# Optimization experiments

Measured on AMD Instinct MI355X. Metric: run time of the kernel, lower is better.

## Reference

```python
import jax, jax.numpy as jnp
import numpy as np

B, F, H, C = 256, 512, 1024, 1000
LN_EPS = 1e-5


def _proj(x, W, b, g, be):
    # AdaptiveAvgPool2d(1) + Flatten + Linear + LayerNorm + GELU(exact)
    p = x.mean(axis=(2, 3))                       # [B, Cin]
    h = p @ W + b                                 # [B, F]
    mu = h.mean(axis=-1, keepdims=True)
    var = h.var(axis=-1, keepdims=True)           # ddof=0, matches torch LayerNorm
    h = (h - mu) / jnp.sqrt(var + LN_EPS) * g + be
    return jax.nn.gelu(h, approximate=False)


def setup_inputs() -> dict:
    key = jax.random.key(0)
    ks = iter(jax.random.split(key, 64))
    def rn(shape, s=1.0):
        return jax.random.normal(next(ks), shape, jnp.float32) * s
    inp = {}
    feats = {"s1": (16, 112), "s2": (24, 56), "s3": (40, 28), "s4": (80, 14), "s5": (160, 7)}
    for n, (c, hw) in feats.items():
        inp[n] = rn((B, c, hw, hw))
    inp["ff"] = rn((B, 960, 7, 7))
    for i, c in enumerate([16, 24, 40, 80, 160], start=1):
        inp[f"Wp{i}"] = rn((c, F), 0.02)
        inp[f"bp{i}"] = jnp.zeros((F,), jnp.float32)
        inp[f"g{i}"] = jnp.ones((F,), jnp.float32)
        inp[f"be{i}"] = jnp.zeros((F,), jnp.float32)
    inp["Wg1"] = rn((960, H), 0.02); inp["bg1"] = jnp.zeros((H,), jnp.float32)
    inp["Wg2"] = rn((H, H // 2), 0.02); inp["bg2"] = jnp.zeros((H // 2,), jnp.float32)
    inp["Wg3"] = rn((H // 2, 5), 0.02); inp["bg3"] = jnp.zeros((5,), jnp.float32)
    inp["Wc1"] = rn((F, H), 0.02); inp["bc1"] = jnp.zeros((H,), jnp.float32)
    inp["Wc2"] = rn((H, H // 2), 0.02); inp["bc2"] = jnp.zeros((H // 2,), jnp.float32)
    inp["Wc3"] = rn((H // 2, C), 0.02); inp["bc3"] = jnp.zeros((C,), jnp.float32)
    return inp


def reference(s1, s2, s3, s4, s5, ff,
              Wp1, bp1, g1, be1, Wp2, bp2, g2, be2, Wp3, bp3, g3, be3,
              Wp4, bp4, g4, be4, Wp5, bp5, g5, be5,
              Wg1, bg1, Wg2, bg2, Wg3, bg3,
              Wc1, bc1, Wc2, bc2, Wc3, bc3):
    # gate on pooled final backbone features (dropout inactive at eval)
    gate_in = ff.mean(axis=(2, 3))                         # [B, 960]
    h = jax.nn.relu(gate_in @ Wg1 + bg1)
    h = jax.nn.relu(h @ Wg2 + bg2)
    gate_logits = h @ Wg3 + bg3                            # [B, 5]

    # per-stage projections -> [B, 5, F]
    stack = jnp.stack([
        _proj(s1, Wp1, bp1, g1, be1),
        _proj(s2, Wp2, bp2, g2, be2),
        _proj(s3, Wp3, bp3, g3, be3),
        _proj(s4, Wp4, bp4, g4, be4),
        _proj(s5, Wp5, bp5, g5, be5),
    ], axis=1)

    topv, topi = jax.lax.top_k(gate_logits, 2)             # [B, 2]
    w = jax.nn.softmax(topv, axis=1)                       # softmax over top-k logits
    sel = jnp.take_along_axis(stack, topi[:, :, None], axis=1)  # [B, 2, F]
    mixture = (sel * w[:, :, None]).sum(axis=1)            # [B, F]

    h = jax.nn.relu(mixture @ Wc1 + bc1)
    h = jax.nn.relu(h @ Wc2 + bc2)
    logits = h @ Wc3 + bc3                                 # [B, C]
    return logits, gate_logits, topi, w
```

## Files before the change

kernel.cpp:

```cpp
#include <hip/hip_runtime.h>
#include <math.h>


struct Pool4Segs {
    const float* src[4];
    float*       dst[4];
    int n4[4];
    int cum[4];
    float inv[4];
};

__global__ __launch_bounds__(256) void pool_big_kernel(Pool4Segs S, int total_waves) {
    int gid  = blockIdx.x * 256 + threadIdx.x;
    int wave = gid >> 6;
    int lane = gid & 63;
    if (wave >= total_waves) return;
    int s = 0;
    #pragma unroll
    for (int i = 0; i < 3; ++i) if (wave >= S.cum[i]) s = i + 1;
    int row = wave - (s == 0 ? 0 : S.cum[s - 1]);
    const int n4 = S.n4[s];
    const float4* p4 = (const float4*)(S.src[s]) + (size_t)row * n4;

    float a0 = 0.f, a1 = 0.f, a2 = 0.f, a3 = 0.f;
    float a4 = 0.f, a5 = 0.f, a6 = 0.f, a7 = 0.f;
    int k = lane;
    for (; k + 448 < n4; k += 512) {
        float4 v0 = p4[k];       float4 v1 = p4[k + 64];
        float4 v2 = p4[k + 128]; float4 v3 = p4[k + 192];
        float4 v4 = p4[k + 256]; float4 v5 = p4[k + 320];
        float4 v6 = p4[k + 384]; float4 v7 = p4[k + 448];
        a0 += (v0.x + v0.y) + (v0.z + v0.w);
        a1 += (v1.x + v1.y) + (v1.z + v1.w);
        a2 += (v2.x + v2.y) + (v2.z + v2.w);
        a3 += (v3.x + v3.y) + (v3.z + v3.w);
        a4 += (v4.x + v4.y) + (v4.z + v4.w);
        a5 += (v5.x + v5.y) + (v5.z + v5.w);
        a6 += (v6.x + v6.y) + (v6.z + v6.w);
        a7 += (v7.x + v7.y) + (v7.z + v7.w);
    }
    for (; k + 192 < n4; k += 256) {
        float4 v0 = p4[k];       float4 v1 = p4[k + 64];
        float4 v2 = p4[k + 128]; float4 v3 = p4[k + 192];
        a0 += (v0.x + v0.y) + (v0.z + v0.w);
        a1 += (v1.x + v1.y) + (v1.z + v1.w);
        a2 += (v2.x + v2.y) + (v2.z + v2.w);
        a3 += (v3.x + v3.y) + (v3.z + v3.w);
    }
    for (; k < n4; k += 64) {
        float4 v = p4[k];
        a0 += (v.x + v.y) + (v.z + v.w);
    }
    float acc = ((a0 + a1) + (a2 + a3)) + ((a4 + a5) + (a6 + a7));
    #pragma unroll
    for (int off = 32; off > 0; off >>= 1) acc += __shfl_down(acc, off, 64);
    if (lane == 0) S.dst[s][row] = acc * S.inv[s];
}

__global__ __launch_bounds__(256) void pool_small_kernel(const float* __restrict__ s5,
        const float* __restrict__ ff, float* __restrict__ dst5, float* __restrict__ dstf,
        int rows5) {
    __shared__ float lds[64 * 49];
    const int tid  = threadIdx.x;
    const int row0 = blockIdx.x * 64;
    const float* src;
    float* dst;
    int rbase;
    if (row0 < rows5) { src = s5; dst = dst5; rbase = row0; }
    else              { src = ff; dst = dstf; rbase = row0 - rows5; }
    const float4* p4 = (const float4*)(src + (size_t)rbase * 49);
    float4* l4 = (float4*)lds;
    float4 v0 = p4[tid];
    float4 v1 = p4[tid + 256];
    float4 v2 = p4[tid + 512];
    float4 v3;
    const bool t3 = (tid < 784 - 768);
    if (t3) v3 = p4[tid + 768];
    l4[tid]       = v0;
    l4[tid + 256] = v1;
    l4[tid + 512] = v2;
    if (t3) l4[tid + 768] = v3;
    __syncthreads();
    const int r  = tid >> 2;
    const int c0 = tid & 3;
    float s = 0.f;
    #pragma unroll
    for (int c = c0; c < 49; c += 4) s += lds[r * 49 + c];
    s += __shfl_down(s, 2, 64);
    s += __shfl_down(s, 1, 64);
    if (c0 == 0) dst[rbase + r] = s * (1.f / 49.f);
}

__global__ __launch_bounds__(256) void fc_tile_kernel(const float* __restrict__ X,
        const float* __restrict__ W, float* __restrict__ P,
        int M, int K, int N, int Kc, int ntiles) {
    __shared__ __align__(16) float Xs[8][68];
    __shared__ __align__(16) float Ws[8][68];
    const int tpk = 4 * ntiles;
    int bid = blockIdx.x;
    int ks  = bid / tpk;
    int rem = bid - ks * tpk;
    int mt  = rem / ntiles;
    int nt  = rem - mt * ntiles;
    const int m0 = mt * 64, n0 = nt * 64;
    const int k0 = ks * Kc;
    int k1 = k0 + Kc; if (k1 > K) k1 = K;

    const int tid = threadIdx.x;
    const int tm = tid & 15;
    const int tn = tid >> 4;
    const int xa = tid >> 3, xb = tid & 7;
    const int wc = tid & 63, wb = tid >> 6;
    const int nw = n0 + wc;
    const bool wok = (nw < N);

    float4 acc[4];
    #pragma unroll
    for (int r = 0; r < 4; ++r) acc[r] = make_float4(0.f, 0.f, 0.f, 0.f);

    float x0, x1, w0v, w1v;
    x0  = X[(size_t)(m0 + xa) * K + k0 + xb];
    x1  = X[(size_t)(m0 + xa + 32) * K + k0 + xb];
    w0v = wok ? W[(size_t)(k0 + wb) * N + nw] : 0.f;
    w1v = wok ? W[(size_t)(k0 + wb + 4) * N + nw] : 0.f;

    for (int kt = k0; kt < k1; kt += 8) {
        __syncthreads();
        Xs[xb][xa] = x0; Xs[xb][xa + 32] = x1;
        Ws[wb][wc] = w0v; Ws[wb + 4][wc] = w1v;
        __syncthreads();
        if (kt + 8 < k1) {
            x0  = X[(size_t)(m0 + xa) * K + kt + 8 + xb];
            x1  = X[(size_t)(m0 + xa + 32) * K + kt + 8 + xb];
            w0v = wok ? W[(size_t)(kt + 8 + wb) * N + nw] : 0.f;
            w1v = wok ? W[(size_t)(kt + 8 + wb + 4) * N + nw] : 0.f;
        }
        #pragma unroll
        for (int kk = 0; kk < 8; ++kk) {
            float4 xr = *(const float4*)&Xs[kk][tm * 4];
            float4 wr = *(const float4*)&Ws[kk][tn * 4];
            acc[0].x += xr.x * wr.x; acc[0].y += xr.x * wr.y;
            acc[0].z += xr.x * wr.z; acc[0].w += xr.x * wr.w;
            acc[1].x += xr.y * wr.x; acc[1].y += xr.y * wr.y;
            acc[1].z += xr.y * wr.z; acc[1].w += xr.y * wr.w;
            acc[2].x += xr.z * wr.x; acc[2].y += xr.z * wr.y;
            acc[2].z += xr.z * wr.z; acc[2].w += xr.z * wr.w;
            acc[3].x += xr.w * wr.x; acc[3].y += xr.w * wr.y;
            acc[3].z += xr.w * wr.z; acc[3].w += xr.w * wr.w;
        }
    }
    const int nbase = n0 + tn * 4;
    #pragma unroll
    for (int r = 0; r < 4; ++r) {
        int row = m0 + tm * 4 + r;
        float* pp = P + ((size_t)ks * M + row) * N + nbase;
        if (nbase + 3 < N) {
            *(float4*)pp = acc[r];
        } else {
            float v[4] = { acc[r].x, acc[r].y, acc[r].z, acc[r].w };
            for (int c = 0; c < 4; ++c) if (nbase + c < N) pp[c] = v[c];
        }
    }
}

__global__ __launch_bounds__(256) void reduce_bias_kernel(const float* __restrict__ P,
        const float* __restrict__ bias, float* __restrict__ Y,
        int MN, int N, int KS, int do_relu) {
    int i = (blockIdx.x * 256 + threadIdx.x) * 4;
    if (i >= MN) return;
    float4 a = *(const float4*)(P + i);
    for (int s = 1; s < KS; ++s) {
        float4 b = *(const float4*)(P + (size_t)s * MN + i);
        a.x += b.x; a.y += b.y; a.z += b.z; a.w += b.w;
    }
    int n = i - (i / N) * N;
    float4 bb = *(const float4*)(bias + n);
    a.x += bb.x; a.y += bb.y; a.z += bb.z; a.w += bb.w;
    if (do_relu) {
        a.x = fmaxf(a.x, 0.f); a.y = fmaxf(a.y, 0.f);
        a.z = fmaxf(a.z, 0.f); a.w = fmaxf(a.w, 0.f);
    }
    *(float4*)(Y + i) = a;
}

struct ProjParams {
    const float* W[5];
    const float* bp[5];
    const float* g[5];
    const float* be[5];
    int K[5];
    int poff[5];
};

__global__ __launch_bounds__(256) void proj_gemm_kernel(ProjParams P,
        const float* __restrict__ pools, float* __restrict__ proj_out) {
    __shared__ __align__(16) float Xs[8][68];
    __shared__ __align__(16) float Ws[8][68];
    const int st = blockIdx.y;
    const int K  = P.K[st];
    const float* X = pools + P.poff[st];
    const float* W = P.W[st];
    const int N = 512;
    int bid = blockIdx.x;
    int mt  = bid >> 3;
    int nt  = bid & 7;
    const int m0 = mt * 64, n0 = nt * 64;

    const int tid = threadIdx.x;
    const int tm = tid & 15;
    const int tn = tid >> 4;
    const int xa = tid >> 3, xb = tid & 7;
    const int wc = tid & 63, wb = tid >> 6;
    const int nw = n0 + wc;

    float4 acc[4];
    #pragma unroll
    for (int r = 0; r < 4; ++r) acc[r] = make_float4(0.f, 0.f, 0.f, 0.f);

    float x0, x1, w0v, w1v;
    x0  = X[(size_t)(m0 + xa) * K + xb];
    x1  = X[(size_t)(m0 + xa + 32) * K + xb];
    w0v = W[(size_t)wb * N + nw];
    w1v = W[(size_t)(wb + 4) * N + nw];

    for (int kt = 0; kt < K; kt += 8) {
        __syncthreads();
        Xs[xb][xa] = x0; Xs[xb][xa + 32] = x1;
        Ws[wb][wc] = w0v; Ws[wb + 4][wc] = w1v;
        __syncthreads();
        if (kt + 8 < K) {
            x0  = X[(size_t)(m0 + xa) * K + kt + 8 + xb];
            x1  = X[(size_t)(m0 + xa + 32) * K + kt + 8 + xb];
            w0v = W[(size_t)(kt + 8 + wb) * N + nw];
            w1v = W[(size_t)(kt + 8 + wb + 4) * N + nw];
        }
        #pragma unroll
        for (int kk = 0; kk < 8; ++kk) {
            float4 xr = *(const float4*)&Xs[kk][tm * 4];
            float4 wr = *(const float4*)&Ws[kk][tn * 4];
            acc[0].x += xr.x * wr.x; acc[0].y += xr.x * wr.y;
            acc[0].z += xr.x * wr.z; acc[0].w += xr.x * wr.w;
            acc[1].x += xr.y * wr.x; acc[1].y += xr.y * wr.y;
            acc[1].z += xr.y * wr.z; acc[1].w += xr.y * wr.w;
            acc[2].x += xr.z * wr.x; acc[2].y += xr.z * wr.y;
            acc[2].z += xr.z * wr.z; acc[2].w += xr.z * wr.w;
            acc[3].x += xr.w * wr.x; acc[3].y += xr.w * wr.y;
            acc[3].z += xr.w * wr.z; acc[3].w += xr.w * wr.w;
        }
    }
    const int nbase = n0 + tn * 4;
    float4 bb = *(const float4*)(P.bp[st] + nbase);
    float* op = proj_out + (size_t)st * 131072 + (size_t)(m0 + tm * 4) * N + nbase;
    #pragma unroll
    for (int r = 0; r < 4; ++r) {
        float4 v = acc[r];
        v.x += bb.x; v.y += bb.y; v.z += bb.z; v.w += bb.w;
        *(float4*)(op + (size_t)r * N) = v;
    }
}

__global__ __launch_bounds__(256) void fc3_top2_kernel(const float* __restrict__ X,
        const float* __restrict__ W, const float* __restrict__ bias,
        int* __restrict__ topi, float* __restrict__ wsm,
        float* __restrict__ out_gl, float* __restrict__ out_topi,
        float* __restrict__ out_w, int K) {
    const int b    = blockIdx.x;
    const int tid  = threadIdx.x;
    const int lane = tid & 63;
    const int wv   = tid >> 6;
    __shared__ float red[4][5];
    const float* x = X + (size_t)b * K;
    float acc[5] = {0.f, 0.f, 0.f, 0.f, 0.f};
    for (int k = tid; k < K; k += 256) {
        float xv = x[k];
        const float* wr = W + (size_t)k * 5;
        acc[0] += xv * wr[0]; acc[1] += xv * wr[1]; acc[2] += xv * wr[2];
        acc[3] += xv * wr[3]; acc[4] += xv * wr[4];
    }
    #pragma unroll
    for (int off = 32; off > 0; off >>= 1) {
        #pragma unroll
        for (int j = 0; j < 5; ++j) acc[j] += __shfl_down(acc[j], off, 64);
    }
    if (lane == 0) {
        #pragma unroll
        for (int j = 0; j < 5; ++j) red[wv][j] = acc[j];
    }
    __syncthreads();
    if (tid == 0) {
        float v[5];
        #pragma unroll
        for (int j = 0; j < 5; ++j)
            v[j] = ((red[0][j] + red[1][j]) + (red[2][j] + red[3][j])) + bias[j];
        int i0 = 0;
        #pragma unroll
        for (int i = 1; i < 5; ++i) if (v[i] > v[i0]) i0 = i;
        int i1 = -1;
        #pragma unroll
        for (int i = 0; i < 5; ++i) {
            if (i == i0) continue;
            if (i1 < 0 || v[i] > v[i1]) i1 = i;
        }
        float e1 = __expf(v[i1] - v[i0]);
        float inv = 1.f / (1.f + e1);
        float w0 = inv, w1 = e1 * inv;
        topi[b * 2] = i0; topi[b * 2 + 1] = i1;
        wsm[b * 2] = w0;  wsm[b * 2 + 1] = w1;
        #pragma unroll
        for (int j = 0; j < 5; ++j) out_gl[b * 5 + j] = v[j];
        out_topi[b * 2]     = (float)i0;
        out_topi[b * 2 + 1] = (float)i1;
        out_w[b * 2]     = w0;
        out_w[b * 2 + 1] = w1;
    }
}

__global__ __launch_bounds__(512) void mixln_kernel(ProjParams P,
        const float* __restrict__ proj_out, const int* __restrict__ topi,
        const float* __restrict__ wsm, float* __restrict__ mix) {
    const int b = blockIdx.x;
    const int f = threadIdx.x;
    __shared__ float redS[8], redQ[8];
    __shared__ float s_mu, s_rstd;

    float acc = 0.f;
    for (int j = 0; j < 2; ++j) {
        __syncthreads();
        const int st = topi[b * 2 + j];
        float h = proj_out[(size_t)st * 131072 + (size_t)b * 512 + f];

        float s = h, q = h * h;
        #pragma unroll
        for (int off = 32; off > 0; off >>= 1) {
            s += __shfl_down(s, off, 64);
            q += __shfl_down(q, off, 64);
        }
        const int lane = threadIdx.x & 63, wid = threadIdx.x >> 6;
        if (lane == 0) { redS[wid] = s; redQ[wid] = q; }
        __syncthreads();
        if (threadIdx.x == 0) {
            float ts = 0.f, tq = 0.f;
            #pragma unroll
            for (int i = 0; i < 8; ++i) { ts += redS[i]; tq += redQ[i]; }
            float mu  = ts * (1.f / 512.f);
            float var = tq * (1.f / 512.f) - mu * mu;
            s_mu   = mu;
            s_rstd = rsqrtf(var + 1e-5f);
        }
        __syncthreads();

        float x  = (h - s_mu) * s_rstd * P.g[st][f] + P.be[st][f];
        float ge = 0.5f * x * (1.f + erff(x * 0.70710678118654752f));
        acc += wsm[b * 2 + j] * ge;
    }
    mix[(size_t)b * 512 + f] = acc;
}

extern "C" void kernel_launch(void* const* d_in, const int* in_sizes, int n_in,
                              void* d_out, int out_size, void* d_ws, size_t ws_size,
                              hipStream_t stream) {
    const int B = 256, F = 512, H = 1024, C = 1000;

    const float* s1 = (const float*)d_in[0];
    const float* s2 = (const float*)d_in[1];
    const float* s3 = (const float*)d_in[2];
    const float* s4 = (const float*)d_in[3];
    const float* s5 = (const float*)d_in[4];
    const float* ff = (const float*)d_in[5];
    const float *Wp[5], *bp[5], *g[5], *be[5];
    for (int i = 0; i < 5; ++i) {
        Wp[i] = (const float*)d_in[6 + 4 * i];
        bp[i] = (const float*)d_in[7 + 4 * i];
        g[i]  = (const float*)d_in[8 + 4 * i];
        be[i] = (const float*)d_in[9 + 4 * i];
    }
    const float* Wg1 = (const float*)d_in[26]; const float* bg1 = (const float*)d_in[27];
    const float* Wg2 = (const float*)d_in[28]; const float* bg2 = (const float*)d_in[29];
    const float* Wg3 = (const float*)d_in[30]; const float* bg3 = (const float*)d_in[31];
    const float* Wc1 = (const float*)d_in[32]; const float* bc1 = (const float*)d_in[33];
    const float* Wc2 = (const float*)d_in[34]; const float* bc2 = (const float*)d_in[35];
    const float* Wc3 = (const float*)d_in[36]; const float* bc3 = (const float*)d_in[37];

    float* ws = (float*)d_ws;
    const int Ks[5]   = {16, 24, 40, 80, 160};
    const int poff[5] = {0, 4096, 10240, 20480, 40960};
    float* pools    = ws;
    float* gate_in  = ws + 81920;
    float* g1h      = ws + 327680;
    float* g2h      = ws + 589824;
    float* wsm      = ws + 722176;
    int*   topi     = (int*)(ws + 722688);
    float* mix      = ws + 723200;
    float* c1h      = ws + 854272;
    float* c2h      = ws + 1116416;
    float* proj_out = ws + 1247488;
    const size_t part_off = 1902848;
    float* partials = ws + part_off;

    float* out      = (float*)d_out;
    float* out_gl   = out + 256000;
    float* out_topi = out + 257280;
    float* out_w    = out + 257792;

    Pool4Segs S;
    {
        const float* srcs[4] = { s1, s2, s3, s4 };
        float* dsts[4] = { pools + poff[0], pools + poff[1], pools + poff[2], pools + poff[3] };
        const int rls[4]  = { 112 * 112, 56 * 56, 28 * 28, 14 * 14 };
        const int rows[4] = { B * 16, B * 24, B * 40, B * 80 };
        int cum = 0;
        for (int i = 0; i < 4; ++i) {
            S.src[i] = srcs[i]; S.dst[i] = dsts[i]; S.n4[i] = rls[i] / 4;
            cum += rows[i]; S.cum[i] = cum; S.inv[i] = 1.f / rls[i];
        }
        int blocks = (cum * 64 + 255) / 256;
        pool_big_kernel<<<blocks, 256, 0, stream>>>(S, cum);
    }
    {
        int rows5 = B * 160;
        int total = rows5 + B * 960;
        pool_small_kernel<<<total / 64, 256, 0, stream>>>(s5, ff, pools + poff[4], gate_in, rows5);
    }

    auto fc = [&](const float* X, const float* W, const float* bias, float* Y,
                  int K, int N, int KSwant, int do_relu) {
        const int M = 256;
        int ntiles = (N + 63) / 64;
        size_t avail = ws_size / 4 > part_off ? ws_size / 4 - part_off : 0;
        int KSmax = (int)(avail / ((size_t)M * N));
        int KS = KSwant; if (KS > KSmax) KS = KSmax; if (KS < 1) KS = 1;
        int Kc = (((K + KS - 1) / KS) + 7) & ~7;
        KS = (K + Kc - 1) / Kc;
        int blocks = KS * 4 * ntiles;
        fc_tile_kernel<<<blocks, 256, 0, stream>>>(X, W, partials, M, K, N, Kc, ntiles);
        int MN = M * N;
        reduce_bias_kernel<<<(MN / 4 + 255) / 256, 256, 0, stream>>>(
            partials, bias, Y, MN, N, KS, do_relu);
    };

    fc(gate_in, Wg1, bg1, g1h, 960, H, 8, 1);
    fc(g1h, Wg2, bg2, g2h, H, H / 2, 16, 1);
    fc3_top2_kernel<<<B, 256, 0, stream>>>(g2h, Wg3, bg3, topi, wsm,
                                           out_gl, out_topi, out_w, H / 2);

    ProjParams P;
    for (int i = 0; i < 5; ++i) {
        P.W[i] = Wp[i]; P.bp[i] = bp[i]; P.g[i] = g[i]; P.be[i] = be[i];
        P.K[i] = Ks[i]; P.poff[i] = poff[i];
    }
    proj_gemm_kernel<<<dim3(32, 5), 256, 0, stream>>>(P, pools, proj_out);
    mixln_kernel<<<B, 512, 0, stream>>>(P, proj_out, topi, wsm, mix);

    fc(mix, Wc1, bc1, c1h, F, H, 8, 1);
    fc(c1h, Wc2, bc2, c2h, H, H / 2, 16, 1);
    fc(c2h, Wc3, bc3, out, H / 2, C, 8, 0);
}
```

Before: 584.7 us.

## Widen FC k-tile to 16 with float4 loads and split pooling launch

The FC tile kernel now stages 16 k-values per iteration instead of 8 and loads X and W with float4 vector loads, halving barrier count per k and improving global load width. The split-K chunk is rounded to multiples of 16 to match. Separately, the big pooling launch is split into two kernels, one for stage 1 (112x112) and one for stages 2-4, so per-row work is more uniform within each launch. This adds one kernel launch, and the X store into transposed LDS may cause bank conflicts.

```diff
diff --git a/kernel.cpp b/kernel.cpp
--- a/kernel.cpp
+++ b/kernel.cpp
@@ -94,8 +94,8 @@
 __global__ __launch_bounds__(256) void fc_tile_kernel(const float* __restrict__ X,
         const float* __restrict__ W, float* __restrict__ P,
         int M, int K, int N, int Kc, int ntiles) {
-    __shared__ __align__(16) float Xs[8][68];
-    __shared__ __align__(16) float Ws[8][68];
+    __shared__ __align__(16) float Xs[16][68];
+    __shared__ __align__(16) float Ws[16][68];
     const int tpk = 4 * ntiles;
     int bid = blockIdx.x;
     int ks  = bid / tpk;
@@ -109,44 +109,56 @@
     const int tid = threadIdx.x;
     const int tm = tid & 15;
     const int tn = tid >> 4;
-    const int xa = tid >> 3, xb = tid & 7;
-    const int wc = tid & 63, wb = tid >> 6;
-    const int nw = n0 + wc;
-    const bool wok = (nw < N);
+    const int xr = tid >> 2, xc = tid & 3;
+    const int wr = tid >> 4, wc = tid & 15;
+    const int nwc = n0 + wc * 4;
 
     float4 acc[4];
     #pragma unroll
     for (int r = 0; r < 4; ++r) acc[r] = make_float4(0.f, 0.f, 0.f, 0.f);
 
-    float x0, x1, w0v, w1v;
-    x0  = X[(size_t)(m0 + xa) * K + k0 + xb];
-    x1  = X[(size_t)(m0 + xa + 32) * K + k0 + xb];
-    w0v = wok ? W[(size_t)(k0 + wb) * N + nw] : 0.f;
-    w1v = wok ? W[(size_t)(k0 + wb + 4) * N + nw] : 0.f;
-
-    for (int kt = k0; kt < k1; kt += 8) {
-        __syncthreads();
-        Xs[xb][xa] = x0; Xs[xb][xa + 32] = x1;
-        Ws[wb][wc] = w0v; Ws[wb + 4][wc] = w1v;
-        __syncthreads();
-        if (kt + 8 < k1) {
-            x0  = X[(size_t)(m0 + xa) * K + kt + 8 + xb];
-            x1  = X[(size_t)(m0 + xa + 32) * K + kt + 8 + xb];
-            w0v = wok ? W[(size_t)(kt + 8 + wb) * N + nw] : 0.f;
-            w1v = wok ? W[(size_t)(kt + 8 + wb + 4) * N + nw] : 0.f;
-        }
-        #pragma unroll
-        for (int kk = 0; kk < 8; ++kk) {
-            float4 xr = *(const float4*)&Xs[kk][tm * 4];
-            float4 wr = *(const float4*)&Ws[kk][tn * 4];
-            acc[0].x += xr.x * wr.x; acc[0].y += xr.x * wr.y;
-            acc[0].z += xr.x * wr.z; acc[0].w += xr.x * wr.w;
-            acc[1].x += xr.y * wr.x; acc[1].y += xr.y * wr.y;
-            acc[1].z += xr.y * wr.z; acc[1].w += xr.y * wr.w;
-            acc[2].x += xr.z * wr.x; acc[2].y += xr.z * wr.y;
-            acc[2].z += xr.z * wr.z; acc[2].w += xr.z * wr.w;
-            acc[3].x += xr.w * wr.x; acc[3].y += xr.w * wr.y;
-            acc[3].z += xr.w * wr.z; acc[3].w += xr.w * wr.w;
+    float4 xv, wv;
+    xv = *(const float4*)(X + (size_t)(m0 + xr) * K + k0 + xc * 4);
+    if (nwc + 3 < N) {
+        wv = *(const float4*)(W + (size_t)(k0 + wr) * N + nwc);
+    } else {
+        wv.x = (nwc + 0 < N) ? W[(size_t)(k0 + wr) * N + nwc + 0] : 0.f;
+        wv.y = (nwc + 1 < N) ? W[(size_t)(k0 + wr) * N + nwc + 1] : 0.f;
+        wv.z = (nwc + 2 < N) ? W[(size_t)(k0 + wr) * N + nwc + 2] : 0.f;
+        wv.w = (nwc + 3 < N) ? W[(size_t)(k0 + wr) * N + nwc + 3] : 0.f;
+    }
+
+    for (int kt = k0; kt < k1; kt += 16) {
+        __syncthreads();
+        Xs[xc * 4 + 0][xr] = xv.x;
+        Xs[xc * 4 + 1][xr] = xv.y;
+        Xs[xc * 4 + 2][xr] = xv.z;
+        Xs[xc * 4 + 3][xr] = xv.w;
+        *(float4*)&Ws[wr][wc * 4] = wv;
+        __syncthreads();
+        if (kt + 16 < k1) {
+            xv = *(const float4*)(X + (size_t)(m0 + xr) * K + kt + 16 + xc * 4);
+            if (nwc + 3 < N) {
+                wv = *(const float4*)(W + (size_t)(kt + 16 + wr) * N + nwc);
+            } else {
+                wv.x = (nwc + 0 < N) ? W[(size_t)(kt + 16 + wr) * N + nwc + 0] : 0.f;
+                wv.y = (nwc + 1 < N) ? W[(size_t)(kt + 16 + wr) * N + nwc + 1] : 0.f;
+                wv.z = (nwc + 2 < N) ? W[(size_t)(kt + 16 + wr) * N + nwc + 2] : 0.f;
+                wv.w = (nwc + 3 < N) ? W[(size_t)(kt + 16 + wr) * N + nwc + 3] : 0.f;
+            }
+        }
+        #pragma unroll
+        for (int kk = 0; kk < 16; ++kk) {
+            float4 xr4 = *(const float4*)&Xs[kk][tm * 4];
+            float4 wr4 = *(const float4*)&Ws[kk][tn * 4];
+            acc[0].x += xr4.x * wr4.x; acc[0].y += xr4.x * wr4.y;
+            acc[0].z += xr4.x * wr4.z; acc[0].w += xr4.x * wr4.w;
+            acc[1].x += xr4.y * wr4.x; acc[1].y += xr4.y * wr4.y;
+            acc[1].z += xr4.y * wr4.z; acc[1].w += xr4.y * wr4.w;
+            acc[2].x += xr4.z * wr4.x; acc[2].y += xr4.z * wr4.y;
+            acc[2].z += xr4.z * wr4.z; acc[2].w += xr4.z * wr4.w;
+            acc[3].x += xr4.w * wr4.x; acc[3].y += xr4.w * wr4.y;
+            acc[3].z += xr4.w * wr4.z; acc[3].w += xr4.w * wr4.w;
         }
     }
     const int nbase = n0 + tn * 4;
@@ -402,19 +414,28 @@
     float* out_topi = out + 257280;
     float* out_w    = out + 257792;
 
-    Pool4Segs S;
     {
-        const float* srcs[4] = { s1, s2, s3, s4 };
-        float* dsts[4] = { pools + poff[0], pools + poff[1], pools + poff[2], pools + poff[3] };
-        const int rls[4]  = { 112 * 112, 56 * 56, 28 * 28, 14 * 14 };
-        const int rows[4] = { B * 16, B * 24, B * 40, B * 80 };
+        Pool4Segs Sa;
+        for (int i = 0; i < 4; ++i) {
+            Sa.src[i] = s1; Sa.dst[i] = pools + poff[0];
+            Sa.n4[i] = 112 * 112 / 4; Sa.cum[i] = B * 16; Sa.inv[i] = 1.f / (112 * 112);
+        }
+        int waves_a = B * 16;
+        pool_big_kernel<<<(waves_a * 64 + 255) / 256, 256, 0, stream>>>(Sa, waves_a);
+
+        Pool4Segs Sb;
+        const float* srcs[3] = { s2, s3, s4 };
+        float* dsts[3] = { pools + poff[1], pools + poff[2], pools + poff[3] };
+        const int rls[3]  = { 56 * 56, 28 * 28, 14 * 14 };
+        const int rows[3] = { B * 24, B * 40, B * 80 };
         int cum = 0;
-        for (int i = 0; i < 4; ++i) {
-            S.src[i] = srcs[i]; S.dst[i] = dsts[i]; S.n4[i] = rls[i] / 4;
-            cum += rows[i]; S.cum[i] = cum; S.inv[i] = 1.f / rls[i];
-        }
-        int blocks = (cum * 64 + 255) / 256;
-        pool_big_kernel<<<blocks, 256, 0, stream>>>(S, cum);
+        for (int i = 0; i < 3; ++i) {
+            Sb.src[i] = srcs[i]; Sb.dst[i] = dsts[i]; Sb.n4[i] = rls[i] / 4;
+            cum += rows[i]; Sb.cum[i] = cum; Sb.inv[i] = 1.f / rls[i];
+        }
+        Sb.src[3] = srcs[2]; Sb.dst[3] = dsts[2]; Sb.n4[3] = rls[2] / 4;
+        Sb.cum[3] = cum; Sb.inv[3] = 1.f / rls[2];
+        pool_big_kernel<<<(cum * 64 + 255) / 256, 256, 0, stream>>>(Sb, cum);
     }
     {
         int rows5 = B * 160;
@@ -429,7 +450,7 @@
         size_t avail = ws_size / 4 > part_off ? ws_size / 4 - part_off : 0;
         int KSmax = (int)(avail / ((size_t)M * N));
         int KS = KSwant; if (KS > KSmax) KS = KSmax; if (KS < 1) KS = 1;
-        int Kc = (((K + KS - 1) / KS) + 7) & ~7;
+        int Kc = (((K + KS - 1) / KS) + 15) & ~15;
         KS = (K + Kc - 1) / Kc;
         int blocks = KS * 4 * ntiles;
         fc_tile_kernel<<<blocks, 256, 0, stream>>>(X, W, partials, M, K, N, Kc, ntiles);
```

Result: faster. 571.9 us (-2.2%).
